# Performance work log

Hardware: AMD Instinct MI355X
Metric: run time of the kernel (lower is better)

The kernel has to match this reference:

```python
import jax, jax.numpy as jnp
import numpy as np

HEADS = 8
DIM_HEADS = 64
M_DIM = 512
X_DIM = 512
MEM_NUM = 512
N = 16384
PERCENT = 0.25
LAY_NUMBER = 2       # outer refinement iterations
CROSS_LAYERS = 2     # layers inside M_cross_layers
EPS = 1e-5


def setup_inputs() -> dict:
    key = jax.random.key(0)
    ks = jax.random.split(key, 8)
    data = jax.random.normal(ks[0], (N, X_DIM), dtype=jnp.float32)
    Memory = jax.random.normal(ks[1], (MEM_NUM, M_DIM), dtype=jnp.float32)
    # to_kv: Linear(X_dim, 2*kv_dim, bias=False); kv_dim = heads*dim_heads
    Wkv = jax.random.normal(ks[2], (X_DIM, 2 * HEADS * DIM_HEADS), dtype=jnp.float32) * 0.02
    # per cross layer: to_q (no bias) and mutl_heads (with bias)
    Wq = jax.random.normal(ks[3], (CROSS_LAYERS, M_DIM, HEADS * DIM_HEADS), dtype=jnp.float32) * 0.02
    Wm = jax.random.normal(ks[4], (CROSS_LAYERS, HEADS * DIM_HEADS, M_DIM), dtype=jnp.float32) * 0.02
    bm = jnp.zeros((CROSS_LAYERS, M_DIM), dtype=jnp.float32)
    return {"data": data, "Memory": Memory, "Wkv": Wkv, "Wq": Wq, "Wm": Wm, "bm": bm, "istest": 0}


def _layer_norm(x):
    # F.layer_norm over last dim, no affine params
    mu = jnp.mean(x, axis=-1, keepdims=True)
    var = jnp.var(x, axis=-1, keepdims=True)
    return (x - mu) * jax.lax.rsqrt(var + EPS)


def _cross_layer(M, X, Wkv, Wq_l, Wm_l, bm_l):
    # cross_att + residual + layernorm (SublayerConnection); FFN is dead code in source
    q = (M @ Wq_l).reshape(MEM_NUM, HEADS, DIM_HEADS).transpose(1, 0, 2)      # [h, m, dh]
    kv = X @ Wkv                                                              # [n, 2*h*dh]
    k, v = jnp.split(kv, 2, axis=-1)
    k = k.reshape(-1, HEADS, DIM_HEADS).transpose(1, 0, 2)                    # [h, n, dh]
    v = v.reshape(-1, HEADS, DIM_HEADS).transpose(1, 0, 2)
    sim = jnp.einsum('hid,hjd->hij', q, k) * (DIM_HEADS ** -0.5)              # [h, m, n]
    att = jax.nn.softmax(sim, axis=-1)
    o = jnp.einsum('hij,hjd->hid', att, v)                                    # [h, m, dh]
    o = o.transpose(1, 0, 2).reshape(MEM_NUM, HEADS * DIM_HEADS)
    out = o @ Wm_l + bm_l                                                     # [m, M_dim]
    return _layer_norm(out + M)


def _cross_layers(M, X, Wkv, Wq, Wm, bm):
    for l in range(CROSS_LAYERS):
        M = _cross_layer(M, X, Wkv, Wq[l], Wm[l], bm[l])
    return M


def _calucate_sim(data, M):
    # per-sample landmark similarity: max scaled dot product against memory rows
    logits = (data @ M.T) * (DIM_HEADS ** -0.5)   # [N, mem]
    return jnp.max(logits, axis=-1)               # [N]


def _calucate_emb(data, M):
    logits = (data @ M.T) * (DIM_HEADS ** -0.5)   # [N, mem]
    logp = jax.nn.log_softmax(logits, axis=-1)
    p = jnp.exp(logp)
    out_ebs = p @ M                               # soft memory readout [N, M_dim]
    result_loss = -jnp.mean(jnp.max(logp, axis=-1))
    lse = jax.scipy.special.logsumexp(logits, axis=-1)
    zloss = jnp.mean(lse ** 2)                    # router-style z-loss
    return out_ebs, result_loss, zloss


def _select(data, sim_M, k):
    _, top_idx = jax.lax.top_k(sim_M, k)
    X = jnp.zeros_like(data)
    return X.at[top_idx].set(data[top_idx])


def reference(data, Memory, Wkv, Wq, Wm, bm, istest):
    M = Memory
    sim_M = _calucate_sim(data, M)
    percent_count = int(data.shape[0] * PERCENT)
    if not istest:
        X = _select(data, sim_M, percent_count)
        for _ in range(LAY_NUMBER):
            M = _cross_layers(M, X, Wkv, Wq, Wm, bm)
            sim_M = _calucate_sim(data, M)
            X = _select(data, sim_M, percent_count)
    out_ebs, result_loss, zloss = _calucate_emb(data, M)
    return (sim_M, out_ebs, result_loss, zloss)
```

## Files before the change

### kernel.cpp

```cpp
#include <hip/hip_runtime.h>
#include <cstdint>

#define N_DATA 16384
#define DIM 512
#define MEM 512
#define KSEL 4096
#define NH 8
#define DH 64
#define KVDIM 1024
#define SCALE 0.125f
#define ZCNT 12288.0f
#define LN_EPS 1e-5f
#define NSPLIT 4

typedef unsigned short u16;
using short8 = __attribute__((ext_vector_type(8))) short;
using f32x4  = __attribute__((ext_vector_type(4))) float;

__device__ __forceinline__ unsigned fenc(float x) {
    unsigned u = __float_as_uint(x);
    return (u & 0x80000000u) ? ~u : (u | 0x80000000u);
}
__device__ __forceinline__ u16 f2bf(float x) {
    unsigned u = __float_as_uint(x);
    u += 0x7fffu + ((u >> 16) & 1u);
    return (u16)(u >> 16);
}
__device__ __forceinline__ float bf2f(u16 h) { return __uint_as_float(((unsigned)h) << 16); }

__device__ __forceinline__ float waveSum(float v) {
#pragma unroll
    for (int o = 32; o > 0; o >>= 1) v += __shfl_down(v, o, 64);
    return v;
}
__device__ __forceinline__ float waveMax(float v) {
#pragma unroll
    for (int o = 32; o > 0; o >>= 1) v = fmaxf(v, __shfl_down(v, o, 64));
    return v;
}
__device__ float blockSum(float v) {
    __shared__ float sh[4];
    __syncthreads();
    v = waveSum(v);
    if ((threadIdx.x & 63) == 0) sh[threadIdx.x >> 6] = v;
    __syncthreads();
    if (threadIdx.x == 0) { float s = sh[0]; for (int i = 1; i < 4; ++i) s += sh[i]; sh[0] = s; }
    __syncthreads();
    return sh[0];
}
__device__ float blockMax(float v) {
    __shared__ float sh[4];
    __syncthreads();
    v = waveMax(v);
    if ((threadIdx.x & 63) == 0) sh[threadIdx.x >> 6] = v;
    __syncthreads();
    if (threadIdx.x == 0) { float s = sh[0]; for (int i = 1; i < 4; ++i) s = fmaxf(s, sh[i]); sh[0] = s; }
    __syncthreads();
    return sh[0];
}

template<int ROWS, int NW, bool GATHER>
__device__ __forceinline__ void stage_tile(const u16* __restrict__ src, int ld, int k0,
                                           int row0, const int* __restrict__ gidx,
                                           u16* lds, int wave)
{
    constexpr int NI = ROWS / 16;
    const int lane = threadIdx.x & 63;
#pragma unroll
    for (int i = wave; i < NI; i += NW) {
        const int ch = i * 64 + lane;
        const int r = ch >> 2, cc = ch & 3;
        int rg = row0 + r;
        if (GATHER) rg = gidx[rg];
        const u16* g = src + (long)rg * ld + k0 + cc * 8;
        u16* l = lds + i * 512;
        __builtin_amdgcn_global_load_lds((const __attribute__((address_space(1))) void*)g,
                                         (__attribute__((address_space(3))) void*)l,
                                         16, 0, 0);
    }
}

template<int WM, int WN, bool GATHER, int EPI, bool BIAS>
__global__ __launch_bounds__(WM * WN * 64)
void mfma_gemm(const u16* __restrict__ A, const u16* __restrict__ B,
               const float* __restrict__ bias, const int* __restrict__ gidx,
               void* __restrict__ Cv, unsigned* __restrict__ simenc,
               int K, int lda, int ldb, int ldc,
               long zsA, long zsB, long zsC, int zdiv, long zsplitC, float alpha)
{
    constexpr int BM = WM * 64, BN = WN * 64, NW = WM * WN;
    __shared__ __align__(16) u16 As[BM * 32];
    __shared__ __align__(16) u16 Bs[BN * 32];

    const int t = threadIdx.x;
    const int wave = t >> 6, lane = t & 63;
    const int wr = wave / WN, wc = wave % WN;
    const int l15 = lane & 15, l4 = lane >> 4;
    const int bm0 = blockIdx.x * BM, bn0 = blockIdx.y * BN;
    const int zs = (int)blockIdx.z % zdiv;
    const int zh = (int)blockIdx.z / zdiv;
    A += (long)zh * zsA;
    B += (long)zh * zsB;

    f32x4 acc[4][4];
#pragma unroll
    for (int i = 0; i < 4; ++i)
#pragma unroll
        for (int j = 0; j < 4; ++j)
#pragma unroll
            for (int r = 0; r < 4; ++r) acc[i][j][r] = 0.f;

    const int Kd = K / zdiv;
    const int kbeg = zs * Kd;
    for (int k0 = kbeg; k0 < kbeg + Kd; k0 += 32) {
        stage_tile<BM, NW, GATHER>(A, lda, k0, bm0, gidx, As, wave);
        stage_tile<BN, NW, false>(B, ldb, k0, bn0, nullptr, Bs, wave);
        __syncthreads();
        short8 a[4], b[4];
#pragma unroll
        for (int fm = 0; fm < 4; ++fm)
            a[fm] = *(const short8*)(As + (wr * 64 + fm * 16 + l15) * 32 + l4 * 8);
#pragma unroll
        for (int fn = 0; fn < 4; ++fn)
            b[fn] = *(const short8*)(Bs + (wc * 64 + fn * 16 + l15) * 32 + l4 * 8);
#pragma unroll
        for (int fm = 0; fm < 4; ++fm)
#pragma unroll
            for (int fn = 0; fn < 4; ++fn)
                acc[fm][fn] = __builtin_amdgcn_mfma_f32_16x16x32_bf16(a[fm], b[fn], acc[fm][fn], 0, 0, 0);
        __syncthreads();
    }

    if (EPI == 2) {
#pragma unroll
        for (int fm = 0; fm < 4; ++fm)
#pragma unroll
            for (int r = 0; r < 4; ++r) {
                float mx = acc[fm][0][r];
#pragma unroll
                for (int fn = 1; fn < 4; ++fn) mx = fmaxf(mx, acc[fm][fn][r]);
#pragma unroll
                for (int o = 8; o >= 1; o >>= 1) mx = fmaxf(mx, __shfl_xor(mx, o, 64));
                if (l15 == 0) {
                    const int row = bm0 + wr * 64 + fm * 16 + l4 * 4 + r;
                    atomicMax(simenc + row, fenc(alpha * mx));
                }
            }
    } else if (EPI == 0) {
        float* C = (float*)Cv + (long)zh * zsC + (long)zs * zsplitC;
#pragma unroll
        for (int fm = 0; fm < 4; ++fm)
#pragma unroll
            for (int fn = 0; fn < 4; ++fn)
#pragma unroll
                for (int r = 0; r < 4; ++r) {
                    const int row = bm0 + wr * 64 + fm * 16 + l4 * 4 + r;
                    const int col = bn0 + wc * 64 + fn * 16 + l15;
                    float v = alpha * acc[fm][fn][r];
                    if (BIAS) v += bias[col];
                    C[(long)row * ldc + col] = v;
                }
    } else {
        u16* C = (u16*)Cv + (long)zh * zsC + (long)zs * zsplitC;
#pragma unroll
        for (int fm = 0; fm < 4; ++fm)
#pragma unroll
            for (int fn = 0; fn < 4; ++fn)
#pragma unroll
                for (int r = 0; r < 4; ++r) {
                    const int row = bm0 + wr * 64 + fm * 16 + l4 * 4 + r;
                    const int col = bn0 + wc * 64 + fn * 16 + l15;
                    float v = alpha * acc[fm][fn][r];
                    if (BIAS) v += bias[col];
                    C[(long)row * ldc + col] = f2bf(v);
                }
    }
}

__global__ __launch_bounds__(256)
void flash_att(const u16* __restrict__ Q, const u16* __restrict__ KV,
               const u16* __restrict__ VT,
               float* __restrict__ oPart, float* __restrict__ mPart,
               float* __restrict__ lPart)
{
    __shared__ __align__(16) u16 Qs[64 * 64];
    __shared__ __align__(16) u16 Ks[64 * 64];
    __shared__ __align__(16) u16 Vs[64 * 64];
    __shared__ __align__(16) u16 Ps[4][16 * 72];

    const int qt = blockIdx.x, h = blockIdx.y, sp = blockIdx.z;
    const int t = threadIdx.x, wave = t >> 6, lane = t & 63;
    const int l15 = lane & 15, l4 = lane >> 4;

    const u16* Qg = Q + (long)(qt * 64) * 512 + h * 64;
    const u16* Kg = KV + ((long)sp * 1024) * 1024 + h * 64;
    const u16* Vg = VT + ((long)h * 64) * 4096 + sp * 1024;

#pragma unroll
    for (int i = wave; i < 8; i += 4) {
        const int ch = i * 64 + lane, r = ch >> 3, s = ch & 7;
        __builtin_amdgcn_global_load_lds(
            (const __attribute__((address_space(1))) void*)(Qg + (long)r * 512 + ((s ^ (r & 7)) * 8)),
            (__attribute__((address_space(3))) void*)(Qs + i * 512), 16, 0, 0);
    }
#pragma unroll
    for (int i = wave; i < 8; i += 4) {
        const int ch = i * 64 + lane, r = ch >> 3, s = ch & 7;
        __builtin_amdgcn_global_load_lds(
            (const __attribute__((address_space(1))) void*)(Kg + (long)r * 1024 + ((s ^ (r & 7)) * 8)),
            (__attribute__((address_space(3))) void*)(Ks + i * 512), 16, 0, 0);
    }
#pragma unroll
    for (int i = wave; i < 8; i += 4) {
        const int ch = i * 64 + lane, r = ch >> 3, s = ch & 7;
        __builtin_amdgcn_global_load_lds(
            (const __attribute__((address_space(1))) void*)(Vg + (long)r * 4096 + ((s ^ (r & 7)) * 8)),
            (__attribute__((address_space(3))) void*)(Vs + i * 512), 16, 0, 0);
    }
    __syncthreads();

    const int qr = wave * 16 + l15;
    short8 qf0 = *(const short8*)(Qs + qr * 64 + ((0 * 4 + l4) ^ (qr & 7)) * 8);
    short8 qf1 = *(const short8*)(Qs + qr * 64 + ((1 * 4 + l4) ^ (qr & 7)) * 8);

    float m = -3.0e38f, lsum = 0.f;
    f32x4 acc_o[4];
#pragma unroll
    for (int nf = 0; nf < 4; ++nf)
#pragma unroll
        for (int r = 0; r < 4; ++r) acc_o[nf][r] = 0.f;

    u16* myP = &Ps[wave][0];

    for (int kt = 0; kt < KSEL / 64 / NSPLIT; ++kt) {
        f32x4 acc_s[4];
#pragma unroll
        for (int mf = 0; mf < 4; ++mf) {
#pragma unroll
            for (int r = 0; r < 4; ++r) acc_s[mf][r] = 0.f;
            const int kr = mf * 16 + l15;
            const short8 ka0 = *(const short8*)(Ks + kr * 64 + ((0 * 4 + l4) ^ (kr & 7)) * 8);
            const short8 ka1 = *(const short8*)(Ks + kr * 64 + ((1 * 4 + l4) ^ (kr & 7)) * 8);
            acc_s[mf] = __builtin_amdgcn_mfma_f32_16x16x32_bf16(ka0, qf0, acc_s[mf], 0, 0, 0);
            acc_s[mf] = __builtin_amdgcn_mfma_f32_16x16x32_bf16(ka1, qf1, acc_s[mf], 0, 0, 0);
        }
        float sv[16];
#pragma unroll
        for (int mf = 0; mf < 4; ++mf)
#pragma unroll
            for (int r = 0; r < 4; ++r) sv[mf * 4 + r] = SCALE * acc_s[mf][r];
        float pm = sv[0];
#pragma unroll
        for (int j = 1; j < 16; ++j) pm = fmaxf(pm, sv[j]);
        pm = fmaxf(pm, __shfl_xor(pm, 16, 64));
        pm = fmaxf(pm, __shfl_xor(pm, 32, 64));
        const float mnew = fmaxf(m, pm);
        const float corr = __expf(m - mnew);
        float rs = 0.f;
#pragma unroll
        for (int j = 0; j < 16; ++j) { sv[j] = __expf(sv[j] - mnew); rs += sv[j]; }
        rs += __shfl_xor(rs, 16, 64);
        rs += __shfl_xor(rs, 32, 64);
        lsum = lsum * corr + rs;
        m = mnew;
        const float cf0 = __shfl(corr, l4 * 4 + 0, 64);
        const float cf1 = __shfl(corr, l4 * 4 + 1, 64);
        const float cf2 = __shfl(corr, l4 * 4 + 2, 64);
        const float cf3 = __shfl(corr, l4 * 4 + 3, 64);
#pragma unroll
        for (int nf = 0; nf < 4; ++nf) {
            acc_o[nf][0] *= cf0; acc_o[nf][1] *= cf1;
            acc_o[nf][2] *= cf2; acc_o[nf][3] *= cf3;
        }
#pragma unroll
        for (int mf = 0; mf < 4; ++mf) {
            ushort4 pw;
            pw.x = f2bf(sv[mf * 4 + 0]); pw.y = f2bf(sv[mf * 4 + 1]);
            pw.z = f2bf(sv[mf * 4 + 2]); pw.w = f2bf(sv[mf * 4 + 3]);
            *(ushort4*)(myP + l15 * 72 + mf * 16 + l4 * 4) = pw;
        }
#pragma unroll
        for (int ks = 0; ks < 2; ++ks) {
            const short8 pa = *(const short8*)(myP + l15 * 72 + ks * 32 + l4 * 8);
#pragma unroll
            for (int nf = 0; nf < 4; ++nf) {
                const int dr = nf * 16 + l15;
                const short8 vb = *(const short8*)(Vs + dr * 64 + ((ks * 4 + l4) ^ (dr & 7)) * 8);
                acc_o[nf] = __builtin_amdgcn_mfma_f32_16x16x32_bf16(pa, vb, acc_o[nf], 0, 0, 0);
            }
        }
        if (kt + 1 < KSEL / 64 / NSPLIT) {
            __syncthreads();
            const u16* Kt = Kg + (long)((kt + 1) * 64) * 1024;
            const u16* Vt = Vg + (kt + 1) * 64;
#pragma unroll
            for (int i = wave; i < 8; i += 4) {
                const int ch = i * 64 + lane, r = ch >> 3, s = ch & 7;
                __builtin_amdgcn_global_load_lds(
                    (const __attribute__((address_space(1))) void*)(Kt + (long)r * 1024 + ((s ^ (r & 7)) * 8)),
                    (__attribute__((address_space(3))) void*)(Ks + i * 512), 16, 0, 0);
            }
#pragma unroll
            for (int i = wave; i < 8; i += 4) {
                const int ch = i * 64 + lane, r = ch >> 3, s = ch & 7;
                __builtin_amdgcn_global_load_lds(
                    (const __attribute__((address_space(1))) void*)(Vt + (long)r * 4096 + ((s ^ (r & 7)) * 8)),
                    (__attribute__((address_space(3))) void*)(Vs + i * 512), 16, 0, 0);
            }
            __syncthreads();
        }
    }

    float* ob = oPart + (((long)sp * NH + h) * 8 + qt) * 4096;
#pragma unroll
    for (int nf = 0; nf < 4; ++nf)
#pragma unroll
        for (int r = 0; r < 4; ++r)
            ob[(wave * 16 + l4 * 4 + r) * 64 + nf * 16 + l15] = acc_o[nf][r];
    if (lane < 16) {
        const int qi = wave * 16 + lane;
        mPart[((sp * NH + h) * 8 + qt) * 64 + qi] = m;
        lPart[((sp * NH + h) * 8 + qt) * 64 + qi] = lsum;
    }
}

__global__ __launch_bounds__(256)
void flash_combine(const float* __restrict__ oPart, const float* __restrict__ mPart,
                   const float* __restrict__ lPart, u16* __restrict__ o_bf)
{
    const int qt = blockIdx.x & 7, h = blockIdx.x >> 3;
    const int t = threadIdx.x;
    const int q = t >> 2, d0 = (t & 3) << 4;
    float mi[NSPLIT], li[NSPLIT];
#pragma unroll
    for (int sp = 0; sp < NSPLIT; ++sp) {
        const int sb = ((sp * NH + h) * 8 + qt) * 64 + q;
        mi[sp] = mPart[sb];
        li[sp] = lPart[sb];
    }
    float ms = 0.f;
#pragma unroll
    for (int sp = 0; sp < NSPLIT; ++sp) ms = fmaxf(ms, mi[sp]);
    float denom = ZCNT * __expf(-ms);
    float f[NSPLIT];
#pragma unroll
    for (int sp = 0; sp < NSPLIT; ++sp) { f[sp] = __expf(mi[sp] - ms); denom += li[sp] * f[sp]; }
    const float inv = 1.f / denom;
    float o[16];
#pragma unroll
    for (int j = 0; j < 16; ++j) o[j] = 0.f;
#pragma unroll
    for (int sp = 0; sp < NSPLIT; ++sp) {
        const float* ob = oPart + (((long)sp * NH + h) * 8 + qt) * 4096 + q * 64 + d0;
        const float fs = f[sp] * inv;
#pragma unroll
        for (int j = 0; j < 16; j += 4) {
            const float4 v = *(const float4*)(ob + j);
            o[j] += fs * v.x; o[j + 1] += fs * v.y; o[j + 2] += fs * v.z; o[j + 3] += fs * v.w;
        }
    }
    u16* op = o_bf + (qt * 64 + q) * 512 + h * 64 + d0;
#pragma unroll
    for (int j = 0; j < 16; j += 4) {
        ushort4 w4;
        w4.x = f2bf(o[j]); w4.y = f2bf(o[j + 1]); w4.z = f2bf(o[j + 2]); w4.w = f2bf(o[j + 3]);
        *(ushort4*)(op + j) = w4;
    }
}

__global__ __launch_bounds__(256)
void conv_f32_bf(const float* __restrict__ s, u16* __restrict__ d, int n)
{
    const int i = (blockIdx.x * 256 + threadIdx.x) * 4;
    if (i >= n) return;
    const float4 v = *(const float4*)(s + i);
    ushort4 o;
    o.x = f2bf(v.x); o.y = f2bf(v.y); o.z = f2bf(v.z); o.w = f2bf(v.w);
    *(ushort4*)(d + i) = o;
}

template<bool INBF>
__global__ __launch_bounds__(256)
void transpose_bf(const void* __restrict__ Sv, u16* __restrict__ D,
                  int Rr, int Cc, int ldS)
{
    __shared__ float tile[32][33];
    const int c0 = blockIdx.x * 32, r0 = blockIdx.y * 32;
    const int tx = threadIdx.x & 31, ty = threadIdx.x >> 5;
#pragma unroll
    for (int j = 0; j < 32; j += 8) {
        const int r = r0 + ty + j, c = c0 + tx;
        float v = INBF ? bf2f(((const u16*)Sv)[(long)r * ldS + c])
                       : ((const float*)Sv)[(long)r * ldS + c];
        tile[ty + j][tx] = v;
    }
    __syncthreads();
#pragma unroll
    for (int j = 0; j < 32; j += 8) {
        const int cO = c0 + ty + j, rO = r0 + tx;
        D[(long)cO * Rr + rO] = f2bf(tile[tx][ty + j]);
    }
}

__device__ __forceinline__ unsigned scan1024_excl(unsigned v, unsigned* wsum)
{
    const int lane = threadIdx.x & 63, wv = threadIdx.x >> 6;
    __syncthreads();
    unsigned x = v;
#pragma unroll
    for (int o = 1; o < 64; o <<= 1) {
        unsigned y = __shfl_up(x, o, 64);
        if (lane >= o) x += y;
    }
    if (lane == 63) wsum[wv] = x;
    __syncthreads();
    if (threadIdx.x < 16) {
        unsigned w2 = wsum[threadIdx.x];
#pragma unroll
        for (int o = 1; o < 16; o <<= 1) {
            unsigned y = __shfl_up(w2, o, 64);
            if ((int)threadIdx.x >= o) w2 += y;
        }
        wsum[threadIdx.x] = w2;
    }
    __syncthreads();
    const unsigned off = (wv > 0) ? wsum[wv - 1] : 0u;
    return off + x - v;
}

#define SEL_T 1024
#define SEL_CH (N_DATA / SEL_T)
__global__ __launch_bounds__(SEL_T)
void select_topk(const unsigned* __restrict__ key, int* __restrict__ idxo, int k)
{
    __shared__ unsigned whist[16][256];
    __shared__ unsigned hist[256];
    __shared__ unsigned wsum[16];
    __shared__ unsigned sh_bin, sh_r;
    const int t = threadIdx.x;
    const int wv = t >> 6;
    const int base = t * SEL_CH;

    unsigned kreg[SEL_CH];
#pragma unroll
    for (int c = 0; c < SEL_CH; ++c) kreg[c] = key[base + c];

    unsigned prefix = 0, mask = 0;
    unsigned r = (unsigned)k;
    for (int p = 3; p >= 0; --p) {
        __syncthreads();
        for (int i = t; i < 16 * 256; i += SEL_T) ((unsigned*)whist)[i] = 0u;
        __syncthreads();
#pragma unroll
        for (int c = 0; c < SEL_CH; ++c) {
            const unsigned kv = kreg[c];
            if ((kv & mask) == prefix)
                atomicAdd(&whist[wv][(kv >> (p * 8)) & 255u], 1u);
        }
        __syncthreads();
        if (t < 256) {
            unsigned s = 0;
#pragma unroll
            for (int wq = 0; wq < 16; ++wq) s += whist[wq][t];
            hist[t] = s;
        }
        __syncthreads();
        if (t < 64) {
            const int b0 = 255 - 4 * t;
            const unsigned c = hist[b0] + hist[b0 - 1] + hist[b0 - 2] + hist[b0 - 3];
            unsigned x = c;
#pragma unroll
            for (int o = 1; o < 64; o <<= 1) {
                unsigned y = __shfl_up(x, o, 64);
                if (t >= o) x += y;
            }
            const unsigned pre = x - c;
            if (pre < r && r <= x) {
                unsigned cum = pre;
#pragma unroll
                for (int j = 0; j < 4; ++j) {
                    const int b = b0 - j;
                    cum += hist[b];
                    if (cum >= r) { sh_bin = (unsigned)b; sh_r = r - (cum - hist[b]); break; }
                }
            }
        }
        __syncthreads();
        prefix |= sh_bin << (p * 8);
        mask |= 255u << (p * 8);
        r = sh_r;
    }
    const unsigned thr = prefix;
    const unsigned ties = r;

    unsigned ceq = 0;
#pragma unroll
    for (int c = 0; c < SEL_CH; ++c) ceq += (kreg[c] == thr) ? 1u : 0u;
    const unsigned eqbase = scan1024_excl(ceq, wsum);
    unsigned eq = eqbase, csel = 0;
#pragma unroll
    for (int c = 0; c < SEL_CH; ++c) {
        const unsigned kv = kreg[c];
        bool s;
        if (kv == thr) { s = (eq < ties); ++eq; }
        else s = (kv > thr);
        csel += s ? 1u : 0u;
    }
    unsigned pos = scan1024_excl(csel, wsum);
    eq = eqbase;
#pragma unroll
    for (int c = 0; c < SEL_CH; ++c) {
        const unsigned kv = kreg[c];
        bool s;
        if (kv == thr) { s = (eq < ties); ++eq; }
        else s = (kv > thr);
        if (s) idxo[pos++] = base + c;
    }
}

__global__ __launch_bounds__(256)
void ln_add_k(const float* __restrict__ outp, const float* __restrict__ Min,
              float* __restrict__ Mout, u16* __restrict__ Mbf)
{
    const int r = blockIdx.x;
    const int t = threadIdx.x;
    float x0 = outp[r * DIM + t] + Min[r * DIM + t];
    float x1 = outp[r * DIM + t + 256] + Min[r * DIM + t + 256];
    float s = blockSum(x0 + x1);
    float s2 = blockSum(x0 * x0 + x1 * x1);
    const float mu = s * (1.f / DIM);
    const float var = s2 * (1.f / DIM) - mu * mu;
    const float rs = rsqrtf(var + LN_EPS);
    const float y0 = (x0 - mu) * rs, y1 = (x1 - mu) * rs;
    Mout[r * DIM + t] = y0;
    Mout[r * DIM + t + 256] = y1;
    Mbf[r * DIM + t] = f2bf(y0);
    Mbf[r * DIM + t + 256] = f2bf(y1);
}

__global__ __launch_bounds__(256)
void emb_softmax_bf(u16* __restrict__ logits, float* __restrict__ simout,
                    float* __restrict__ lse, float* __restrict__ mlp)
{
    const int r = blockIdx.x;
    u16* row = logits + (long)r * MEM;
    const int t = threadIdx.x;
    unsigned w = *(const unsigned*)(row + 2 * t);
    float a = bf2f((u16)(w & 0xffffu)), b = bf2f((u16)(w >> 16));
    float mx = blockMax(fmaxf(a, b));
    float s = blockSum(__expf(a - mx) + __expf(b - mx));
    float l = mx + __logf(s);
    if (t == 0) { simout[r] = mx; lse[r] = l; mlp[r] = mx - l; }
    unsigned o = (unsigned)f2bf(__expf(a - l)) | ((unsigned)f2bf(__expf(b - l)) << 16);
    *(unsigned*)(row + 2 * t) = o;
}

__global__ __launch_bounds__(256)
void reduce_loss(const float* __restrict__ lse, const float* __restrict__ mlp,
                 float* __restrict__ o2)
{
    const int t = threadIdx.x;
    float s1 = 0.f, s2 = 0.f;
    for (int i = t; i < N_DATA; i += 256) { s1 += mlp[i]; float l = lse[i]; s2 += l * l; }
    s1 = blockSum(s1);
    s2 = blockSum(s2);
    if (t == 0) { o2[0] = -s1 * (1.f / N_DATA); o2[1] = s2 * (1.f / N_DATA); }
}

extern "C" void kernel_launch(void* const* d_in, const int* in_sizes, int n_in,
                              void* d_out, int out_size, void* d_ws, size_t ws_size,
                              hipStream_t stream)
{
    (void)in_sizes; (void)n_in; (void)out_size; (void)ws_size;
    const float* data   = (const float*)d_in[0];
    const float* Memory = (const float*)d_in[1];
    const float* Wkv    = (const float*)d_in[2];
    const float* Wq     = (const float*)d_in[3];
    const float* Wm     = (const float*)d_in[4];
    const float* bm     = (const float*)d_in[5];
    float* out = (float*)d_out;

    char* w = (char*)d_ws;
    unsigned* simenc = (unsigned*)(w + 0);
    int*   idx     = (int*)  (w + 65536);
    float* lse     = (float*)(w + 81920);
    float* mlp     = (float*)(w + 147456);
    float* Ma      = (float*)(w + 262144);
    float* Mb      = (float*)(w + 1310720);
    u16*   Mbf0    = (u16*)  (w + 2359296);
    u16*   MT_bf   = (u16*)  (w + 2883584);
    u16*   WqT_bf  = (u16*)  (w + 3407872);
    u16*   WmT_bf  = (u16*)  (w + 4456448);
    u16*   WkvT_bf = (u16*)  (w + 5505024);
    u16*   q_bf    = (u16*)  (w + 6553600);
    u16*   o_bf    = (u16*)  (w + 7077888);
    float* outp    = (float*)(w + 7602176);
    u16*   data_bf = (u16*)  (w + 8650752);
    u16*   kvsel_bf= (u16*)  (w + 25427968);
    u16*   vT_bf   = (u16*)  (w + 33816576);
    float* oPart   = (float*)(w + 38010880);
    float* mPart   = (float*)(w + 42205184);
    float* lPart   = (float*)(w + 42270720);
    u16*   att_bf  = (u16*)  (w + 54788096);
    u16*   Mbfa    = (u16*)  (w + 88342528);
    u16*   Mbfb    = (u16*)  (w + 88866816);
    u16*   logits_bf = att_bf;

    conv_f32_bf<<<(N_DATA * DIM / 4 + 255) / 256, 256, 0, stream>>>(data, data_bf, N_DATA * DIM);
    conv_f32_bf<<<(DIM * DIM / 4 + 255) / 256, 256, 0, stream>>>(Memory, Mbf0, DIM * DIM);
    transpose_bf<false><<<dim3(KVDIM / 32, DIM / 32), 256, 0, stream>>>(Wkv, WkvT_bf, DIM, KVDIM, KVDIM);
    for (int l = 0; l < 2; ++l) {
        transpose_bf<false><<<dim3(16, 16), 256, 0, stream>>>(Wq + (long)l * DIM * DIM, WqT_bf + (long)l * DIM * DIM, DIM, DIM, DIM);
        transpose_bf<false><<<dim3(16, 16), 256, 0, stream>>>(Wm + (long)l * DIM * DIM, WmT_bf + (long)l * DIM * DIM, DIM, DIM, DIM);
    }

    auto sim_select_kv = [&](const u16* Mrows_bf) {
        hipMemsetAsync(simenc, 0, N_DATA * 4, stream);
        mfma_gemm<2, 2, false, 2, false><<<dim3(128, 4, 1), 256, 0, stream>>>(
            data_bf, Mrows_bf, nullptr, nullptr, nullptr, simenc,
            DIM, DIM, DIM, 0, 0, 0, 0, 1, 0, SCALE);
        select_topk<<<1, SEL_T, 0, stream>>>(simenc, idx, KSEL);
        mfma_gemm<2, 2, true, 1, false><<<dim3(32, 8, 1), 256, 0, stream>>>(
            data_bf, WkvT_bf, nullptr, idx, kvsel_bf, nullptr,
            DIM, DIM, DIM, KVDIM, 0, 0, 0, 1, 0, 1.0f);
        transpose_bf<true><<<dim3(DIM / 32, KSEL / 32), 256, 0, stream>>>(
            kvsel_bf + DIM, vT_bf, KSEL, DIM, KVDIM);
    };

    auto cross = [&](const float* Mcur, const u16* Mcur_bf, float* Mnext, u16* Mnext_bf, int l) {
        mfma_gemm<2, 2, false, 1, false><<<dim3(4, 4, 1), 256, 0, stream>>>(
            Mcur_bf, WqT_bf + (long)l * DIM * DIM, nullptr, nullptr, q_bf, nullptr,
            DIM, DIM, DIM, DIM, 0, 0, 0, 1, 0, 1.0f);
        flash_att<<<dim3(8, NH, NSPLIT), 256, 0, stream>>>(q_bf, kvsel_bf, vT_bf, oPart, mPart, lPart);
        flash_combine<<<64, 256, 0, stream>>>(oPart, mPart, lPart, o_bf);
        mfma_gemm<2, 2, false, 0, true><<<dim3(4, 4, 1), 256, 0, stream>>>(
            o_bf, WmT_bf + (long)l * DIM * DIM, bm + (long)l * DIM, nullptr, outp, nullptr,
            DIM, DIM, DIM, DIM, 0, 0, 0, 1, 0, 1.0f);
        ln_add_k<<<DIM, 256, 0, stream>>>(outp, Mcur, Mnext, Mnext_bf);
    };

    const float* Mcur = Memory;
    const u16*  curbf = Mbf0;
    float* Mnext = Ma;
    u16*   nextbf = Mbfa;
    sim_select_kv(curbf);
    for (int it = 0; it < 2; ++it) {
        for (int l = 0; l < 2; ++l) {
            cross(Mcur, curbf, Mnext, nextbf, l);
            Mcur = Mnext; curbf = nextbf;
            Mnext = (Mcur == Ma) ? Mb : Ma;
            nextbf = (curbf == Mbfa) ? Mbfb : Mbfa;
        }
        if (it == 0) sim_select_kv(curbf);
    }

    mfma_gemm<2, 2, false, 1, false><<<dim3(128, 4, 1), 256, 0, stream>>>(
        data_bf, curbf, nullptr, nullptr, logits_bf, nullptr,
        DIM, DIM, DIM, MEM, 0, 0, 0, 1, 0, SCALE);
    emb_softmax_bf<<<N_DATA, 256, 0, stream>>>(logits_bf, out, lse, mlp);
    transpose_bf<false><<<dim3(16, 16), 256, 0, stream>>>(Mcur, MT_bf, MEM, DIM, DIM);
    mfma_gemm<2, 2, false, 0, false><<<dim3(128, 4, 1), 256, 0, stream>>>(
        logits_bf, MT_bf, nullptr, nullptr, out + N_DATA, nullptr,
        MEM, MEM, MEM, DIM, 0, 0, 0, 1, 0, 1.0f);
    reduce_loss<<<1, 256, 0, stream>>>(lse, mlp, out + N_DATA + (long)N_DATA * DIM);
}
```

Before: 418.5 us.

## Fuse row reductions into full-row GEMM kernels and double-buffer flash attention KV

Adds a full-row GEMM kernel (64 rows x 512 cols per block, 8 waves) whose epilogue does the row max, the residual-add layernorm, or the softmax/logsumexp in-block. It replaces the atomic-max sim epilogue plus memset, the separate ln_add_k kernel and the emb_softmax kernel, cutting launches and logits round-trips. Flash attention now double-buffers K/V tiles so the next tile's load overlaps compute, and the four weight transposes merge into one launch. The row-GEMM uses only 8 blocks for the 512-row cases and 256 blocks for the data GEMMs, which may lower occupancy.

```diff
diff --git a/kernel.cpp b/kernel.cpp
--- a/kernel.cpp
+++ b/kernel.cpp
@@ -33,11 +33,6 @@
     for (int o = 32; o > 0; o >>= 1) v += __shfl_down(v, o, 64);
     return v;
 }
-__device__ __forceinline__ float waveMax(float v) {
-#pragma unroll
-    for (int o = 32; o > 0; o >>= 1) v = fmaxf(v, __shfl_down(v, o, 64));
-    return v;
-}
 __device__ float blockSum(float v) {
     __shared__ float sh[4];
     __syncthreads();
@@ -45,16 +40,6 @@
     if ((threadIdx.x & 63) == 0) sh[threadIdx.x >> 6] = v;
     __syncthreads();
     if (threadIdx.x == 0) { float s = sh[0]; for (int i = 1; i < 4; ++i) s += sh[i]; sh[0] = s; }
-    __syncthreads();
-    return sh[0];
-}
-__device__ float blockMax(float v) {
-    __shared__ float sh[4];
-    __syncthreads();
-    v = waveMax(v);
-    if ((threadIdx.x & 63) == 0) sh[threadIdx.x >> 6] = v;
-    __syncthreads();
-    if (threadIdx.x == 0) { float s = sh[0]; for (int i = 1; i < 4; ++i) s = fmaxf(s, sh[i]); sh[0] = s; }
     __syncthreads();
     return sh[0];
 }
@@ -131,22 +116,7 @@
         __syncthreads();
     }
 
-    if (EPI == 2) {
-#pragma unroll
-        for (int fm = 0; fm < 4; ++fm)
-#pragma unroll
-            for (int r = 0; r < 4; ++r) {
-                float mx = acc[fm][0][r];
-#pragma unroll
-                for (int fn = 1; fn < 4; ++fn) mx = fmaxf(mx, acc[fm][fn][r]);
-#pragma unroll
-                for (int o = 8; o >= 1; o >>= 1) mx = fmaxf(mx, __shfl_xor(mx, o, 64));
-                if (l15 == 0) {
-                    const int row = bm0 + wr * 64 + fm * 16 + l4 * 4 + r;
-                    atomicMax(simenc + row, fenc(alpha * mx));
-                }
-            }
-    } else if (EPI == 0) {
+    if (EPI == 0) {
         float* C = (float*)Cv + (long)zh * zsC + (long)zs * zsplitC;
 #pragma unroll
         for (int fm = 0; fm < 4; ++fm)
@@ -175,6 +145,186 @@
                     C[(long)row * ldc + col] = f2bf(v);
                 }
     }
+    (void)simenc;
+}
+
+template<int EPI>
+__global__ __launch_bounds__(512)
+void mfma_gemm_row(const u16* __restrict__ A, const u16* __restrict__ B,
+                   const float* __restrict__ bias, const float* __restrict__ Min,
+                   unsigned* __restrict__ simenc,
+                   float* __restrict__ Mout, u16* __restrict__ Obf,
+                   float* __restrict__ simf, float* __restrict__ lse,
+                   float* __restrict__ mlp, float alpha)
+{
+    __shared__ __align__(16) u16 As[64 * 32];
+    __shared__ __align__(16) u16 Bs[512 * 32];
+    const int t = threadIdx.x, wave = t >> 6, lane = t & 63;
+    const int wc = wave;
+    const int l15 = lane & 15, l4 = lane >> 4;
+    const int bm0 = blockIdx.x * 64;
+
+    f32x4 acc[4][4];
+#pragma unroll
+    for (int i = 0; i < 4; ++i)
+#pragma unroll
+        for (int j = 0; j < 4; ++j)
+#pragma unroll
+            for (int r = 0; r < 4; ++r) acc[i][j][r] = 0.f;
+
+    for (int k0 = 0; k0 < 512; k0 += 32) {
+        stage_tile<64, 8, false>(A, 512, k0, bm0, nullptr, As, wave);
+        stage_tile<512, 8, false>(B, 512, k0, 0, nullptr, Bs, wave);
+        __syncthreads();
+        short8 a[4], b[4];
+#pragma unroll
+        for (int fm = 0; fm < 4; ++fm)
+            a[fm] = *(const short8*)(As + (fm * 16 + l15) * 32 + l4 * 8);
+#pragma unroll
+        for (int fn = 0; fn < 4; ++fn)
+            b[fn] = *(const short8*)(Bs + (wc * 64 + fn * 16 + l15) * 32 + l4 * 8);
+#pragma unroll
+        for (int fm = 0; fm < 4; ++fm)
+#pragma unroll
+            for (int fn = 0; fn < 4; ++fn)
+                acc[fm][fn] = __builtin_amdgcn_mfma_f32_16x16x32_bf16(a[fm], b[fn], acc[fm][fn], 0, 0, 0);
+        __syncthreads();
+    }
+
+    float* red  = (float*)As;
+    float* red2 = red + 512;
+    float* rowv = (float*)Bs;
+
+    if (EPI == 0) {
+#pragma unroll
+        for (int fm = 0; fm < 4; ++fm)
+#pragma unroll
+            for (int r = 0; r < 4; ++r) {
+                float mx = alpha * acc[fm][0][r];
+#pragma unroll
+                for (int fn = 1; fn < 4; ++fn) mx = fmaxf(mx, alpha * acc[fm][fn][r]);
+#pragma unroll
+                for (int o = 1; o <= 8; o <<= 1) mx = fmaxf(mx, __shfl_xor(mx, o, 64));
+                if (l15 == 0) red[(fm * 16 + l4 * 4 + r) * 8 + wc] = mx;
+            }
+        __syncthreads();
+        if (t < 64) {
+            float mx = red[t * 8];
+#pragma unroll
+            for (int j = 1; j < 8; ++j) mx = fmaxf(mx, red[t * 8 + j]);
+            simenc[bm0 + t] = fenc(mx);
+        }
+    } else if (EPI == 1) {
+        float v[4][4][4];
+#pragma unroll
+        for (int fm = 0; fm < 4; ++fm)
+#pragma unroll
+            for (int fn = 0; fn < 4; ++fn) {
+                const int col = wc * 64 + fn * 16 + l15;
+                const float bi = bias[col];
+#pragma unroll
+                for (int r = 0; r < 4; ++r) {
+                    const int row = bm0 + fm * 16 + l4 * 4 + r;
+                    v[fm][fn][r] = acc[fm][fn][r] + bi + Min[(long)row * 512 + col];
+                }
+            }
+#pragma unroll
+        for (int fm = 0; fm < 4; ++fm)
+#pragma unroll
+            for (int r = 0; r < 4; ++r) {
+                float s = 0.f, s2 = 0.f;
+#pragma unroll
+                for (int fn = 0; fn < 4; ++fn) { const float x = v[fm][fn][r]; s += x; s2 += x * x; }
+#pragma unroll
+                for (int o = 1; o <= 8; o <<= 1) { s += __shfl_xor(s, o, 64); s2 += __shfl_xor(s2, o, 64); }
+                if (l15 == 0) {
+                    red [(fm * 16 + l4 * 4 + r) * 8 + wc] = s;
+                    red2[(fm * 16 + l4 * 4 + r) * 8 + wc] = s2;
+                }
+            }
+        __syncthreads();
+        if (t < 64) {
+            float s = 0.f, s2 = 0.f;
+#pragma unroll
+            for (int j = 0; j < 8; ++j) { s += red[t * 8 + j]; s2 += red2[t * 8 + j]; }
+            const float mu = s * (1.f / 512.f);
+            const float var = s2 * (1.f / 512.f) - mu * mu;
+            rowv[t] = mu;
+            rowv[64 + t] = rsqrtf(var + LN_EPS);
+        }
+        __syncthreads();
+#pragma unroll
+        for (int fm = 0; fm < 4; ++fm)
+#pragma unroll
+            for (int r = 0; r < 4; ++r) {
+                const int rl = fm * 16 + l4 * 4 + r;
+                const float mu = rowv[rl], rs = rowv[64 + rl];
+#pragma unroll
+                for (int fn = 0; fn < 4; ++fn) {
+                    const int col = wc * 64 + fn * 16 + l15;
+                    const float y = (v[fm][fn][r] - mu) * rs;
+                    Mout[(long)(bm0 + rl) * 512 + col] = y;
+                    Obf [(long)(bm0 + rl) * 512 + col] = f2bf(y);
+                }
+            }
+    } else {
+#pragma unroll
+        for (int fm = 0; fm < 4; ++fm)
+#pragma unroll
+            for (int r = 0; r < 4; ++r) {
+                float mx = alpha * acc[fm][0][r];
+#pragma unroll
+                for (int fn = 1; fn < 4; ++fn) mx = fmaxf(mx, alpha * acc[fm][fn][r]);
+#pragma unroll
+                for (int o = 1; o <= 8; o <<= 1) mx = fmaxf(mx, __shfl_xor(mx, o, 64));
+                if (l15 == 0) red[(fm * 16 + l4 * 4 + r) * 8 + wc] = mx;
+            }
+        __syncthreads();
+        if (t < 64) {
+            float mx = red[t * 8];
+#pragma unroll
+            for (int j = 1; j < 8; ++j) mx = fmaxf(mx, red[t * 8 + j]);
+            rowv[t] = mx;
+        }
+        __syncthreads();
+#pragma unroll
+        for (int fm = 0; fm < 4; ++fm)
+#pragma unroll
+            for (int r = 0; r < 4; ++r) {
+                const int rl = fm * 16 + l4 * 4 + r;
+                const float m = rowv[rl];
+                float s = 0.f;
+#pragma unroll
+                for (int fn = 0; fn < 4; ++fn) s += __expf(alpha * acc[fm][fn][r] - m);
+#pragma unroll
+                for (int o = 1; o <= 8; o <<= 1) s += __shfl_xor(s, o, 64);
+                if (l15 == 0) red[rl * 8 + wc] = s;
+            }
+        __syncthreads();
+        if (t < 64) {
+            float s = 0.f;
+#pragma unroll
+            for (int j = 0; j < 8; ++j) s += red[t * 8 + j];
+            const float m = rowv[t];
+            const float l = m + __logf(s);
+            const int gr = bm0 + t;
+            simf[gr] = m; lse[gr] = l; mlp[gr] = m - l;
+            rowv[64 + t] = l;
+        }
+        __syncthreads();
+#pragma unroll
+        for (int fm = 0; fm < 4; ++fm)
+#pragma unroll
+            for (int r = 0; r < 4; ++r) {
+                const int rl = fm * 16 + l4 * 4 + r;
+                const float l = rowv[64 + rl];
+#pragma unroll
+                for (int fn = 0; fn < 4; ++fn) {
+                    const int col = wc * 64 + fn * 16 + l15;
+                    Obf[(long)(bm0 + rl) * 512 + col] = f2bf(__expf(alpha * acc[fm][fn][r] - l));
+                }
+            }
+    }
 }
 
 __global__ __launch_bounds__(256)
@@ -184,8 +334,8 @@
                float* __restrict__ lPart)
 {
     __shared__ __align__(16) u16 Qs[64 * 64];
-    __shared__ __align__(16) u16 Ks[64 * 64];
-    __shared__ __align__(16) u16 Vs[64 * 64];
+    __shared__ __align__(16) u16 Ks[2][64 * 64];
+    __shared__ __align__(16) u16 Vs[2][64 * 64];
     __shared__ __align__(16) u16 Ps[4][16 * 72];
 
     const int qt = blockIdx.x, h = blockIdx.y, sp = blockIdx.z;
@@ -195,6 +345,25 @@
     const u16* Qg = Q + (long)(qt * 64) * 512 + h * 64;
     const u16* Kg = KV + ((long)sp * 1024) * 1024 + h * 64;
     const u16* Vg = VT + ((long)h * 64) * 4096 + sp * 1024;
+
+    auto stageKV = [&](int kt, int buf) {
+        const u16* Kt = Kg + (long)(kt * 64) * 1024;
+        const u16* Vt = Vg + kt * 64;
+#pragma unroll
+        for (int i = wave; i < 8; i += 4) {
+            const int ch = i * 64 + lane, r = ch >> 3, s = ch & 7;
+            __builtin_amdgcn_global_load_lds(
+                (const __attribute__((address_space(1))) void*)(Kt + (long)r * 1024 + ((s ^ (r & 7)) * 8)),
+                (__attribute__((address_space(3))) void*)(Ks[buf] + i * 512), 16, 0, 0);
+        }
+#pragma unroll
+        for (int i = wave; i < 8; i += 4) {
+            const int ch = i * 64 + lane, r = ch >> 3, s = ch & 7;
+            __builtin_amdgcn_global_load_lds(
+                (const __attribute__((address_space(1))) void*)(Vt + (long)r * 4096 + ((s ^ (r & 7)) * 8)),
+                (__attribute__((address_space(3))) void*)(Vs[buf] + i * 512), 16, 0, 0);
+        }
+    };
 
 #pragma unroll
     for (int i = wave; i < 8; i += 4) {
@@ -203,20 +372,7 @@
             (const __attribute__((address_space(1))) void*)(Qg + (long)r * 512 + ((s ^ (r & 7)) * 8)),
             (__attribute__((address_space(3))) void*)(Qs + i * 512), 16, 0, 0);
     }
-#pragma unroll
-    for (int i = wave; i < 8; i += 4) {
-        const int ch = i * 64 + lane, r = ch >> 3, s = ch & 7;
-        __builtin_amdgcn_global_load_lds(
-            (const __attribute__((address_space(1))) void*)(Kg + (long)r * 1024 + ((s ^ (r & 7)) * 8)),
-            (__attribute__((address_space(3))) void*)(Ks + i * 512), 16, 0, 0);
-    }
-#pragma unroll
-    for (int i = wave; i < 8; i += 4) {
-        const int ch = i * 64 + lane, r = ch >> 3, s = ch & 7;
-        __builtin_amdgcn_global_load_lds(
-            (const __attribute__((address_space(1))) void*)(Vg + (long)r * 4096 + ((s ^ (r & 7)) * 8)),
-            (__attribute__((address_space(3))) void*)(Vs + i * 512), 16, 0, 0);
-    }
+    stageKV(0, 0);
     __syncthreads();
 
     const int qr = wave * 16 + l15;
@@ -231,16 +387,21 @@
         for (int r = 0; r < 4; ++r) acc_o[nf][r] = 0.f;
 
     u16* myP = &Ps[wave][0];
-
-    for (int kt = 0; kt < KSEL / 64 / NSPLIT; ++kt) {
+    constexpr int NT = KSEL / 64 / NSPLIT;
+    int cur = 0;
+
+    for (int kt = 0; kt < NT; ++kt) {
+        if (kt + 1 < NT) stageKV(kt + 1, cur ^ 1);
+        const u16* Kc = Ks[cur];
+        const u16* Vc = Vs[cur];
         f32x4 acc_s[4];
 #pragma unroll
         for (int mf = 0; mf < 4; ++mf) {
 #pragma unroll
             for (int r = 0; r < 4; ++r) acc_s[mf][r] = 0.f;
             const int kr = mf * 16 + l15;
-            const short8 ka0 = *(const short8*)(Ks + kr * 64 + ((0 * 4 + l4) ^ (kr & 7)) * 8);
-            const short8 ka1 = *(const short8*)(Ks + kr * 64 + ((1 * 4 + l4) ^ (kr & 7)) * 8);
+            const short8 ka0 = *(const short8*)(Kc + kr * 64 + ((0 * 4 + l4) ^ (kr & 7)) * 8);
+            const short8 ka1 = *(const short8*)(Kc + kr * 64 + ((1 * 4 + l4) ^ (kr & 7)) * 8);
             acc_s[mf] = __builtin_amdgcn_mfma_f32_16x16x32_bf16(ka0, qf0, acc_s[mf], 0, 0, 0);
             acc_s[mf] = __builtin_amdgcn_mfma_f32_16x16x32_bf16(ka1, qf1, acc_s[mf], 0, 0, 0);
         }
@@ -285,30 +446,12 @@
 #pragma unroll
             for (int nf = 0; nf < 4; ++nf) {
                 const int dr = nf * 16 + l15;
-                const short8 vb = *(const short8*)(Vs + dr * 64 + ((ks * 4 + l4) ^ (dr & 7)) * 8);
+                const short8 vb = *(const short8*)(Vc + dr * 64 + ((ks * 4 + l4) ^ (dr & 7)) * 8);
                 acc_o[nf] = __builtin_amdgcn_mfma_f32_16x16x32_bf16(pa, vb, acc_o[nf], 0, 0, 0);
             }
         }
-        if (kt + 1 < KSEL / 64 / NSPLIT) {
-            __syncthreads();
-            const u16* Kt = Kg + (long)((kt + 1) * 64) * 1024;
-            const u16* Vt = Vg + (kt + 1) * 64;
-#pragma unroll
-            for (int i = wave; i < 8; i += 4) {
-                const int ch = i * 64 + lane, r = ch >> 3, s = ch & 7;
-                __builtin_amdgcn_global_load_lds(
-                    (const __attribute__((address_space(1))) void*)(Kt + (long)r * 1024 + ((s ^ (r & 7)) * 8)),
-                    (__attribute__((address_space(3))) void*)(Ks + i * 512), 16, 0, 0);
-            }
-#pragma unroll
-            for (int i = wave; i < 8; i += 4) {
-                const int ch = i * 64 + lane, r = ch >> 3, s = ch & 7;
-                __builtin_amdgcn_global_load_lds(
-                    (const __attribute__((address_space(1))) void*)(Vt + (long)r * 4096 + ((s ^ (r & 7)) * 8)),
-                    (__attribute__((address_space(3))) void*)(Vs + i * 512), 16, 0, 0);
-            }
-            __syncthreads();
-        }
+        __syncthreads();
+        cur ^= 1;
     }
 
     float* ob = oPart + (((long)sp * NH + h) * 8 + qt) * 4096;
@@ -400,6 +543,25 @@
         const int cO = c0 + ty + j, rO = r0 + tx;
         D[(long)cO * Rr + rO] = f2bf(tile[tx][ty + j]);
     }
+}
+
+__global__ __launch_bounds__(256)
+void transpose_w4(const float* __restrict__ Wq, const float* __restrict__ Wm,
+                  u16* __restrict__ WqT, u16* __restrict__ WmT)
+{
+    const int z = blockIdx.z;
+    const float* S = (z < 2) ? (Wq + (long)z * DIM * DIM) : (Wm + (long)(z - 2) * DIM * DIM);
+    u16* D = (z < 2) ? (WqT + (long)z * DIM * DIM) : (WmT + (long)(z - 2) * DIM * DIM);
+    __shared__ float tile[32][33];
+    const int c0 = blockIdx.x * 32, r0 = blockIdx.y * 32;
+    const int tx = threadIdx.x & 31, ty = threadIdx.x >> 5;
+#pragma unroll
+    for (int j = 0; j < 32; j += 8)
+        tile[ty + j][tx] = S[(long)(r0 + ty + j) * DIM + c0 + tx];
+    __syncthreads();
+#pragma unroll
+    for (int j = 0; j < 32; j += 8)
+        D[(long)(c0 + ty + j) * DIM + r0 + tx] = f2bf(tile[tx][ty + j]);
 }
 
 __device__ __forceinline__ unsigned scan1024_excl(unsigned v, unsigned* wsum)
@@ -516,43 +678,6 @@
         else s = (kv > thr);
         if (s) idxo[pos++] = base + c;
     }
-}
-
-__global__ __launch_bounds__(256)
-void ln_add_k(const float* __restrict__ outp, const float* __restrict__ Min,
-              float* __restrict__ Mout, u16* __restrict__ Mbf)
-{
-    const int r = blockIdx.x;
-    const int t = threadIdx.x;
-    float x0 = outp[r * DIM + t] + Min[r * DIM + t];
-    float x1 = outp[r * DIM + t + 256] + Min[r * DIM + t + 256];
-    float s = blockSum(x0 + x1);
-    float s2 = blockSum(x0 * x0 + x1 * x1);
-    const float mu = s * (1.f / DIM);
-    const float var = s2 * (1.f / DIM) - mu * mu;
-    const float rs = rsqrtf(var + LN_EPS);
-    const float y0 = (x0 - mu) * rs, y1 = (x1 - mu) * rs;
-    Mout[r * DIM + t] = y0;
-    Mout[r * DIM + t + 256] = y1;
-    Mbf[r * DIM + t] = f2bf(y0);
-    Mbf[r * DIM + t + 256] = f2bf(y1);
-}
-
-__global__ __launch_bounds__(256)
-void emb_softmax_bf(u16* __restrict__ logits, float* __restrict__ simout,
-                    float* __restrict__ lse, float* __restrict__ mlp)
-{
-    const int r = blockIdx.x;
-    u16* row = logits + (long)r * MEM;
-    const int t = threadIdx.x;
-    unsigned w = *(const unsigned*)(row + 2 * t);
-    float a = bf2f((u16)(w & 0xffffu)), b = bf2f((u16)(w >> 16));
-    float mx = blockMax(fmaxf(a, b));
-    float s = blockSum(__expf(a - mx) + __expf(b - mx));
-    float l = mx + __logf(s);
-    if (t == 0) { simout[r] = mx; lse[r] = l; mlp[r] = mx - l; }
-    unsigned o = (unsigned)f2bf(__expf(a - l)) | ((unsigned)f2bf(__expf(b - l)) << 16);
-    *(unsigned*)(row + 2 * t) = o;
 }
 
 __global__ __launch_bounds__(256)
@@ -594,31 +719,25 @@
     u16*   WkvT_bf = (u16*)  (w + 5505024);
     u16*   q_bf    = (u16*)  (w + 6553600);
     u16*   o_bf    = (u16*)  (w + 7077888);
-    float* outp    = (float*)(w + 7602176);
     u16*   data_bf = (u16*)  (w + 8650752);
     u16*   kvsel_bf= (u16*)  (w + 25427968);
     u16*   vT_bf   = (u16*)  (w + 33816576);
     float* oPart   = (float*)(w + 38010880);
     float* mPart   = (float*)(w + 42205184);
     float* lPart   = (float*)(w + 42270720);
-    u16*   att_bf  = (u16*)  (w + 54788096);
+    u16*   logits_bf = (u16*)(w + 54788096);
     u16*   Mbfa    = (u16*)  (w + 88342528);
     u16*   Mbfb    = (u16*)  (w + 88866816);
-    u16*   logits_bf = att_bf;
 
     conv_f32_bf<<<(N_DATA * DIM / 4 + 255) / 256, 256, 0, stream>>>(data, data_bf, N_DATA * DIM);
     conv_f32_bf<<<(DIM * DIM / 4 + 255) / 256, 256, 0, stream>>>(Memory, Mbf0, DIM * DIM);
     transpose_bf<false><<<dim3(KVDIM / 32, DIM / 32), 256, 0, stream>>>(Wkv, WkvT_bf, DIM, KVDIM, KVDIM);
-    for (int l = 0; l < 2; ++l) {
-        transpose_bf<false><<<dim3(16, 16), 256, 0, stream>>>(Wq + (long)l * DIM * DIM, WqT_bf + (long)l * DIM * DIM, DIM, DIM, DIM);
-        transpose_bf<false><<<dim3(16, 16), 256, 0, stream>>>(Wm + (long)l * DIM * DIM, WmT_bf + (long)l * DIM * DIM, DIM, DIM, DIM);
-    }
+    transpose_w4<<<dim3(16, 16, 4), 256, 0, stream>>>(Wq, Wm, WqT_bf, WmT_bf);
 
     auto sim_select_kv = [&](const u16* Mrows_bf) {
-        hipMemsetAsync(simenc, 0, N_DATA * 4, stream);
-        mfma_gemm<2, 2, false, 2, false><<<dim3(128, 4, 1), 256, 0, stream>>>(
-            data_bf, Mrows_bf, nullptr, nullptr, nullptr, simenc,
-            DIM, DIM, DIM, 0, 0, 0, 0, 1, 0, SCALE);
+        mfma_gemm_row<0><<<N_DATA / 64, 512, 0, stream>>>(
+            data_bf, Mrows_bf, nullptr, nullptr, simenc,
+            nullptr, nullptr, nullptr, nullptr, nullptr, SCALE);
         select_topk<<<1, SEL_T, 0, stream>>>(simenc, idx, KSEL);
         mfma_gemm<2, 2, true, 1, false><<<dim3(32, 8, 1), 256, 0, stream>>>(
             data_bf, WkvT_bf, nullptr, idx, kvsel_bf, nullptr,
@@ -633,10 +752,9 @@
             DIM, DIM, DIM, DIM, 0, 0, 0, 1, 0, 1.0f);
         flash_att<<<dim3(8, NH, NSPLIT), 256, 0, stream>>>(q_bf, kvsel_bf, vT_bf, oPart, mPart, lPart);
         flash_combine<<<64, 256, 0, stream>>>(oPart, mPart, lPart, o_bf);
-        mfma_gemm<2, 2, false, 0, true><<<dim3(4, 4, 1), 256, 0, stream>>>(
-            o_bf, WmT_bf + (long)l * DIM * DIM, bm + (long)l * DIM, nullptr, outp, nullptr,
-            DIM, DIM, DIM, DIM, 0, 0, 0, 1, 0, 1.0f);
-        ln_add_k<<<DIM, 256, 0, stream>>>(outp, Mcur, Mnext, Mnext_bf);
+        mfma_gemm_row<1><<<DIM / 64, 512, 0, stream>>>(
+            o_bf, WmT_bf + (long)l * DIM * DIM, bm + (long)l * DIM, Mcur, nullptr,
+            Mnext, Mnext_bf, nullptr, nullptr, nullptr, 1.0f);
     };
 
     const float* Mcur = Memory;
@@ -654,10 +772,9 @@
         if (it == 0) sim_select_kv(curbf);
     }
 
-    mfma_gemm<2, 2, false, 1, false><<<dim3(128, 4, 1), 256, 0, stream>>>(
-        data_bf, curbf, nullptr, nullptr, logits_bf, nullptr,
-        DIM, DIM, DIM, MEM, 0, 0, 0, 1, 0, SCALE);
-    emb_softmax_bf<<<N_DATA, 256, 0, stream>>>(logits_bf, out, lse, mlp);
+    mfma_gemm_row<2><<<N_DATA / 64, 512, 0, stream>>>(
+        data_bf, curbf, nullptr, nullptr, nullptr,
+        nullptr, logits_bf, out, lse, mlp, SCALE);
     transpose_bf<false><<<dim3(16, 16), 256, 0, stream>>>(Mcur, MT_bf, MEM, DIM, DIM);
     mfma_gemm<2, 2, false, 0, false><<<dim3(128, 4, 1), 256, 0, stream>>>(
         logits_bf, MT_bf, nullptr, nullptr, out + N_DATA, nullptr,
```

Result: slower. 445.5 us (+6.5%).
